# Kernel optimization log

Hardware: AMD Instinct MI355X
Metric: run time of the kernel (lower is better)

The kernel has to match this reference:

```python
import jax, jax.numpy as jnp
import numpy as np


def setup_inputs() -> dict:
    key = jax.random.key(0)
    k1, k2 = jax.random.split(key)
    B, N, d = 8, 4096, 256
    S_pred = jax.random.normal(k1, (B, N, d), dtype=jnp.float32)
    # binary adjacency in {0,1}; nonzero entries define neighbors
    adjacency = jax.random.randint(k2, (N, N), 0, 2, dtype=jnp.int32)
    return {"S_pred": S_pred, "adjacency": adjacency}


def reference(S_pred, adjacency):
    # S_pred: (B, N, d), adjacency: (N, N)
    B, N, d = S_pred.shape
    A = (adjacency != 0).astype(S_pred.dtype)          # (N, N) binary
    deg = A.sum(axis=1)                                 # (N,) neighbor counts
    # neighbor mean: (A @ S) / deg  -> per node i, mean over j in N(i) of S_j
    neigh_sum = jnp.einsum('ij,bjd->bid', A, S_pred)   # (B, N, d)
    neigh_mean = neigh_sum / jnp.maximum(deg, 1.0)[None, :, None]
    # div_i = mean_j (S_j - S_i) = neigh_mean_i - S_i; zero for isolated nodes
    div = neigh_mean - S_pred                           # (B, N, d)
    mask = (deg > 0).astype(S_pred.dtype)[None, :, None]
    divergence = jnp.sum((div * mask) ** 2) / (B * N * d)
    return divergence
```

## Files before the change

kernel.cpp:

```cpp
#include <hip/hip_runtime.h>
#include <stdint.h>

#define N_NODES 4096
#define DMODEL  256
#define BATCH   8
#define NCOL    (BATCH * DMODEL)
#define KDIM    N_NODES
#define INV_BND (1.0f / 8388608.0f)

typedef __attribute__((ext_vector_type(8))) int   int32x8;
typedef __attribute__((ext_vector_type(4))) float f32x4;

__device__ __forceinline__ void async_load16(const void* g, void* l) {
  __builtin_amdgcn_global_load_lds(
      (const __attribute__((address_space(1))) void*)g,
      (__attribute__((address_space(3))) void*)l, 16, 0, 0);
}

__device__ __forceinline__ f32x4 mfma_mx(int32x8 a, int32x8 b, f32x4 c) {
  return __builtin_amdgcn_mfma_scale_f32_16x16x128_f8f6f4(
      a, b, c, 0, 0, 0, 0x7F7F7F7Fu, 0, 0x7F7F7F7Fu);
}

__global__ __launch_bounds__(256) void fat_prep(const int* __restrict__ adj,
                                                const float* __restrict__ S,
                                                unsigned char* __restrict__ A8,
                                                unsigned char* __restrict__ B8,
                                                float* __restrict__ w,
                                                float* __restrict__ out) {
  __shared__ float tile[64][36];
  __shared__ int wred[4];
  const int bx = blockIdx.x;
  const int t  = threadIdx.x;

  if (bx < N_NODES) {
    if (bx == 0 && t == 0) *out = 0.0f;
    const int4* arow = (const int4*)(adj + (size_t)bx * N_NODES);
    int cnt = 0;
    unsigned int b[4];
#pragma unroll
    for (int q = 0; q < 4; ++q) {
      int4 a = arow[t * 4 + q];
      unsigned int p = 0;
      p |= a.x ? 0x38u       : 0u; cnt += (a.x != 0);
      p |= a.y ? 0x3800u     : 0u; cnt += (a.y != 0);
      p |= a.z ? 0x380000u   : 0u; cnt += (a.z != 0);
      p |= a.w ? 0x38000000u : 0u; cnt += (a.w != 0);
      b[q] = p;
    }
    uint4 o; o.x = b[0]; o.y = b[1]; o.z = b[2]; o.w = b[3];
    ((uint4*)(A8 + (size_t)bx * N_NODES))[t] = o;
#pragma unroll
    for (int off = 32; off > 0; off >>= 1) cnt += __shfl_down(cnt, off);
    if ((t & 63) == 0) wred[t >> 6] = cnt;
    __syncthreads();
    if (t == 0) {
      int total = wred[0] + wred[1] + wred[2] + wred[3];
      w[bx] = (total > 0) ? (1.0f / (float)total) : 0.0f;
    }
  } else {
    const int bt = bx - N_NODES;
    const int j0 = (bt & 63) * 64;
    const int d0 = ((bt >> 6) & 7) * 32;
    const int bb = bt >> 9;
    const float* Sb = S + (size_t)bb * (N_NODES * DMODEL);

    const int c  = t & 7;
    const int jr = t >> 3;
#pragma unroll
    for (int p = 0; p < 2; ++p) {
      const int j = jr + p * 32;
      float4 v = *(const float4*)&Sb[(size_t)(j0 + j) * DMODEL + d0 + c * 4];
      *(float4*)&tile[j][c * 4] = v;
    }
    __syncthreads();

    const int dr = t >> 3;
    const int jt = (t & 7) * 8;
    int lo = __builtin_amdgcn_cvt_pk_fp8_f32(tile[jt + 0][dr], tile[jt + 1][dr], 0, false);
    lo     = __builtin_amdgcn_cvt_pk_fp8_f32(tile[jt + 2][dr], tile[jt + 3][dr], lo, true);
    int hi = __builtin_amdgcn_cvt_pk_fp8_f32(tile[jt + 4][dr], tile[jt + 5][dr], 0, false);
    hi     = __builtin_amdgcn_cvt_pk_fp8_f32(tile[jt + 6][dr], tile[jt + 7][dr], hi, true);
    uint2 o; o.x = (unsigned int)lo; o.y = (unsigned int)hi;
    *(uint2*)&B8[(size_t)(bb * DMODEL + d0 + dr) * KDIM + j0 + jt] = o;
  }
}

__global__ __launch_bounds__(512, 4) void gemm_div(const unsigned char* __restrict__ A8,
                                                   const unsigned char* __restrict__ B8,
                                                   const float* __restrict__ w,
                                                   const float* __restrict__ S,
                                                   float* __restrict__ out) {
  __shared__ unsigned char lds[65536];
  __shared__ float wsum[4];

  const int tid  = threadIdx.x;
  const int lane = tid & 63;
  const int wave = tid >> 6;
  const int grp  = wave >> 2;
  const int w4   = wave & 3;
  const int wm   = w4 >> 1;
  const int wn   = w4 & 1;
  const int l16  = lane & 15;
  const int quad = lane >> 4;

  unsigned char* As = lds + grp * 16384;
  unsigned char* Bs = lds + 32768 + grp * 16384;

  const int rowBase = blockIdx.x * 128;
  const int colBase = blockIdx.y * 128;

  const int srow = lane >> 3;
  const int kc   = ((lane & 7) ^ srow) * 16;

  f32x4 acc[4][4];
  const f32x4 zero = {0.f, 0.f, 0.f, 0.f};
#pragma unroll
  for (int i = 0; i < 4; ++i)
#pragma unroll
    for (int j = 0; j < 4; ++j) acc[i][j] = zero;

  const unsigned char* Ag = A8 + (size_t)rowBase * KDIM;
  const unsigned char* Bg = B8 + (size_t)colBase * KDIM;

  for (int k0 = grp * 128; k0 < KDIM; k0 += 256) {
#pragma unroll
    for (int c = 0; c < 4; ++c) {
      const int r = (w4 * 4 + c) * 8 + srow;
      async_load16(Ag + (size_t)r * KDIM + k0 + kc, As + (w4 * 4 + c) * 1024);
      async_load16(Bg + (size_t)r * KDIM + k0 + kc, Bs + (w4 * 4 + c) * 1024);
    }
    __syncthreads();

    int32x8 bfrag[4];
#pragma unroll
    for (int nt = 0; nt < 4; ++nt) {
      const int r = wn * 64 + nt * 16 + l16;
      const unsigned char* rp = Bs + r * 128;
      const int x = r & 7;
      int4 lo = *(const int4*)(rp + (((2 * quad)    ) ^ x) * 16);
      int4 hi = *(const int4*)(rp + (((2 * quad) | 1) ^ x) * 16);
      bfrag[nt][0] = lo.x; bfrag[nt][1] = lo.y; bfrag[nt][2] = lo.z; bfrag[nt][3] = lo.w;
      bfrag[nt][4] = hi.x; bfrag[nt][5] = hi.y; bfrag[nt][6] = hi.z; bfrag[nt][7] = hi.w;
    }
#pragma unroll
    for (int mt = 0; mt < 4; ++mt) {
      const int r = wm * 64 + mt * 16 + l16;
      const unsigned char* rp = As + r * 128;
      const int x = r & 7;
      int4 lo = *(const int4*)(rp + (((2 * quad)    ) ^ x) * 16);
      int4 hi = *(const int4*)(rp + (((2 * quad) | 1) ^ x) * 16);
      int32x8 a;
      a[0] = lo.x; a[1] = lo.y; a[2] = lo.z; a[3] = lo.w;
      a[4] = hi.x; a[5] = hi.y; a[6] = hi.z; a[7] = hi.w;
#pragma unroll
      for (int nt = 0; nt < 4; ++nt)
        acc[mt][nt] = mfma_mx(a, bfrag[nt], acc[mt][nt]);
    }
    __syncthreads();
  }

  float* stash = (float*)lds;
  if (grp == 1) {
#pragma unroll
    for (int mt = 0; mt < 4; ++mt)
#pragma unroll
      for (int nt = 0; nt < 4; ++nt)
#pragma unroll
        for (int r = 0; r < 4; ++r)
          stash[w4 * 4096 + (mt * 4 + nt) * 256 + (quad * 4 + r) * 16 + l16] =
              acc[mt][nt][r];
  }
  __syncthreads();

  float local = 0.0f;
  if (grp == 0) {
#pragma unroll
    for (int mt = 0; mt < 4; ++mt) {
      const int i0 = rowBase + wm * 64 + mt * 16 + quad * 4;
      float wr[4];
#pragma unroll
      for (int r = 0; r < 4; ++r) wr[r] = w[i0 + r];
#pragma unroll
      for (int nt = 0; nt < 4; ++nt) {
        const int col = colBase + wn * 64 + nt * 16 + l16;
        const int bb = col >> 8;
        const int dd = col & 255;
        const float* Sp = S + (size_t)bb * (N_NODES * DMODEL) + (size_t)i0 * DMODEL + dd;
#pragma unroll
        for (int r = 0; r < 4; ++r) {
          float cs = acc[mt][nt][r] +
                     stash[w4 * 4096 + (mt * 4 + nt) * 256 + (quad * 4 + r) * 16 + l16];
          float v = cs * wr[r] - Sp[(size_t)r * DMODEL];
          v = (wr[r] > 0.0f) ? v : 0.0f;
          local += v * v;
        }
      }
    }
#pragma unroll
    for (int off = 32; off > 0; off >>= 1) local += __shfl_down(local, off);
    if (lane == 0) wsum[w4] = local;
  }
  __syncthreads();
  if (tid == 0)
    atomicAdd(out, (wsum[0] + wsum[1] + wsum[2] + wsum[3]) * INV_BND);
}

extern "C" void kernel_launch(void* const* d_in, const int* in_sizes, int n_in,
                              void* d_out, int out_size, void* d_ws, size_t ws_size,
                              hipStream_t stream) {
  const float* S  = (const float*)d_in[0];
  const int* adj  = (const int*)d_in[1];
  float* out = (float*)d_out;

  unsigned char* A8 = (unsigned char*)d_ws;
  unsigned char* B8 = (unsigned char*)d_ws + (size_t)N_NODES * N_NODES;
  float* w = (float*)((char*)d_ws + (size_t)N_NODES * N_NODES + (size_t)NCOL * KDIM);

  fat_prep<<<N_NODES + N_NODES / 64 * (DMODEL / 32) * BATCH, 256, 0, stream>>>(
      adj, S, A8, B8, w, out);

  gemm_div<<<dim3(N_NODES / 128, NCOL / 128, 1), 512, 0, stream>>>(A8, B8, w, S, out);
}
```

Measured before the change: 165.3 us.

## Remove intra-block split-K in FP8 GEMM and widen prep transpose tiles

The GEMM kernel drops its two-group split-K, where 8 waves each handled half of K and the halves were reduced through LDS. It now runs 4 waves over the full K with a 32KB LDS footprint, which removes the stash write, an extra barrier and LDS usage. The prep transpose now handles 128 rows per block and writes 16-byte FP8 stores instead of 8-byte ones. In exchange, each GEMM block runs twice as many serial K iterations with fewer resident waves per CU, which can reduce latency hiding on a 512-block grid.

```diff
diff --git a/kernel.cpp b/kernel.cpp
--- a/kernel.cpp
+++ b/kernel.cpp
@@ -28,7 +28,7 @@
                                                 unsigned char* __restrict__ B8,
                                                 float* __restrict__ w,
                                                 float* __restrict__ out) {
-  __shared__ float tile[64][36];
+  __shared__ float tile[128][36];
   __shared__ int wred[4];
   const int bx = blockIdx.x;
   const int t  = threadIdx.x;
@@ -60,53 +60,57 @@
     }
   } else {
     const int bt = bx - N_NODES;
-    const int j0 = (bt & 63) * 64;
-    const int d0 = ((bt >> 6) & 7) * 32;
-    const int bb = bt >> 9;
+    const int j0 = (bt & 31) * 128;
+    const int d0 = ((bt >> 5) & 7) * 32;
+    const int bb = bt >> 8;
     const float* Sb = S + (size_t)bb * (N_NODES * DMODEL);
 
-    const int c  = t & 7;
-    const int jr = t >> 3;
-#pragma unroll
-    for (int p = 0; p < 2; ++p) {
-      const int j = jr + p * 32;
+#pragma unroll
+    for (int p = 0; p < 4; ++p) {
+      const int idx = p * 256 + t;
+      const int j = idx >> 3;
+      const int c = idx & 7;
       float4 v = *(const float4*)&Sb[(size_t)(j0 + j) * DMODEL + d0 + c * 4];
       *(float4*)&tile[j][c * 4] = v;
     }
     __syncthreads();
 
     const int dr = t >> 3;
-    const int jt = (t & 7) * 8;
-    int lo = __builtin_amdgcn_cvt_pk_fp8_f32(tile[jt + 0][dr], tile[jt + 1][dr], 0, false);
-    lo     = __builtin_amdgcn_cvt_pk_fp8_f32(tile[jt + 2][dr], tile[jt + 3][dr], lo, true);
-    int hi = __builtin_amdgcn_cvt_pk_fp8_f32(tile[jt + 4][dr], tile[jt + 5][dr], 0, false);
-    hi     = __builtin_amdgcn_cvt_pk_fp8_f32(tile[jt + 6][dr], tile[jt + 7][dr], hi, true);
-    uint2 o; o.x = (unsigned int)lo; o.y = (unsigned int)hi;
-    *(uint2*)&B8[(size_t)(bb * DMODEL + d0 + dr) * KDIM + j0 + jt] = o;
+    const int jt = (t & 7) * 16;
+    uint4 o;
+    {
+      int v0 = __builtin_amdgcn_cvt_pk_fp8_f32(tile[jt + 0][dr], tile[jt + 1][dr], 0, false);
+      v0     = __builtin_amdgcn_cvt_pk_fp8_f32(tile[jt + 2][dr], tile[jt + 3][dr], v0, true);
+      int v1 = __builtin_amdgcn_cvt_pk_fp8_f32(tile[jt + 4][dr], tile[jt + 5][dr], 0, false);
+      v1     = __builtin_amdgcn_cvt_pk_fp8_f32(tile[jt + 6][dr], tile[jt + 7][dr], v1, true);
+      int v2 = __builtin_amdgcn_cvt_pk_fp8_f32(tile[jt + 8][dr], tile[jt + 9][dr], 0, false);
+      v2     = __builtin_amdgcn_cvt_pk_fp8_f32(tile[jt +10][dr], tile[jt +11][dr], v2, true);
+      int v3 = __builtin_amdgcn_cvt_pk_fp8_f32(tile[jt +12][dr], tile[jt +13][dr], 0, false);
+      v3     = __builtin_amdgcn_cvt_pk_fp8_f32(tile[jt +14][dr], tile[jt +15][dr], v3, true);
+      o.x = (unsigned int)v0; o.y = (unsigned int)v1;
+      o.z = (unsigned int)v2; o.w = (unsigned int)v3;
+    }
+    *(uint4*)&B8[(size_t)(bb * DMODEL + d0 + dr) * KDIM + j0 + jt] = o;
   }
 }
 
-__global__ __launch_bounds__(512, 4) void gemm_div(const unsigned char* __restrict__ A8,
+__global__ __launch_bounds__(256, 4) void gemm_div(const unsigned char* __restrict__ A8,
                                                    const unsigned char* __restrict__ B8,
                                                    const float* __restrict__ w,
                                                    const float* __restrict__ S,
                                                    float* __restrict__ out) {
-  __shared__ unsigned char lds[65536];
+  __shared__ unsigned char As[16384];
+  __shared__ unsigned char Bs[16384];
   __shared__ float wsum[4];
 
   const int tid  = threadIdx.x;
   const int lane = tid & 63;
   const int wave = tid >> 6;
-  const int grp  = wave >> 2;
-  const int w4   = wave & 3;
-  const int wm   = w4 >> 1;
-  const int wn   = w4 & 1;
+  const int wm   = wave >> 1;
+  const int wn   = wave & 1;
   const int l16  = lane & 15;
   const int quad = lane >> 4;
 
-  unsigned char* As = lds + grp * 16384;
-  unsigned char* Bs = lds + 32768 + grp * 16384;
-
   const int rowBase = blockIdx.x * 128;
   const int colBase = blockIdx.y * 128;
 
@@ -123,12 +127,13 @@
   const unsigned char* Ag = A8 + (size_t)rowBase * KDIM;
   const unsigned char* Bg = B8 + (size_t)colBase * KDIM;
 
-  for (int k0 = grp * 128; k0 < KDIM; k0 += 256) {
+  for (int k0 = 0; k0 < KDIM; k0 += 128) {
 #pragma unroll
     for (int c = 0; c < 4; ++c) {
-      const int r = (w4 * 4 + c) * 8 + srow;
-      async_load16(Ag + (size_t)r * KDIM + k0 + kc, As + (w4 * 4 + c) * 1024);
-      async_load16(Bg + (size_t)r * KDIM + k0 + kc, Bs + (w4 * 4 + c) * 1024);
+      const int ch = wave * 4 + c;
+      const int r  = ch * 8 + srow;
+      async_load16(Ag + (size_t)r * KDIM + k0 + kc, As + ch * 1024);
+      async_load16(Bg + (size_t)r * KDIM + k0 + kc, Bs + ch * 1024);
     }
     __syncthreads();
 
@@ -160,47 +165,31 @@
     __syncthreads();
   }
 
-  float* stash = (float*)lds;
-  if (grp == 1) {
-#pragma unroll
-    for (int mt = 0; mt < 4; ++mt)
-#pragma unroll
-      for (int nt = 0; nt < 4; ++nt)
-#pragma unroll
-        for (int r = 0; r < 4; ++r)
-          stash[w4 * 4096 + (mt * 4 + nt) * 256 + (quad * 4 + r) * 16 + l16] =
-              acc[mt][nt][r];
+  float local = 0.0f;
+#pragma unroll
+  for (int mt = 0; mt < 4; ++mt) {
+    const int i0 = rowBase + wm * 64 + mt * 16 + quad * 4;
+    float wr[4];
+#pragma unroll
+    for (int r = 0; r < 4; ++r) wr[r] = w[i0 + r];
+#pragma unroll
+    for (int nt = 0; nt < 4; ++nt) {
+      const int col = colBase + wn * 64 + nt * 16 + l16;
+      const int bb = col >> 8;
+      const int dd = col & 255;
+      const float* Sp = S + (size_t)bb * (N_NODES * DMODEL) + (size_t)i0 * DMODEL + dd;
+#pragma unroll
+      for (int r = 0; r < 4; ++r) {
+        float v = acc[mt][nt][r] * wr[r] - Sp[(size_t)r * DMODEL];
+        v = (wr[r] > 0.0f) ? v : 0.0f;
+        local += v * v;
+      }
+    }
   }
-  __syncthreads();
-
-  float local = 0.0f;
-  if (grp == 0) {
-#pragma unroll
-    for (int mt = 0; mt < 4; ++mt) {
-      const int i0 = rowBase + wm * 64 + mt * 16 + quad * 4;
-      float wr[4];
-#pragma unroll
-      for (int r = 0; r < 4; ++r) wr[r] = w[i0 + r];
-#pragma unroll
-      for (int nt = 0; nt < 4; ++nt) {
-        const int col = colBase + wn * 64 + nt * 16 + l16;
-        const int bb = col >> 8;
-        const int dd = col & 255;
-        const float* Sp = S + (size_t)bb * (N_NODES * DMODEL) + (size_t)i0 * DMODEL + dd;
-#pragma unroll
-        for (int r = 0; r < 4; ++r) {
-          float cs = acc[mt][nt][r] +
-                     stash[w4 * 4096 + (mt * 4 + nt) * 256 + (quad * 4 + r) * 16 + l16];
-          float v = cs * wr[r] - Sp[(size_t)r * DMODEL];
-          v = (wr[r] > 0.0f) ? v : 0.0f;
-          local += v * v;
-        }
-      }
-    }
-#pragma unroll
-    for (int off = 32; off > 0; off >>= 1) local += __shfl_down(local, off);
-    if (lane == 0) wsum[w4] = local;
-  }
+
+#pragma unroll
+  for (int off = 32; off > 0; off >>= 1) local += __shfl_down(local, off);
+  if (lane == 0) wsum[wave] = local;
   __syncthreads();
   if (tid == 0)
     atomicAdd(out, (wsum[0] + wsum[1] + wsum[2] + wsum[3]) * INV_BND);
@@ -217,8 +206,8 @@
   unsigned char* B8 = (unsigned char*)d_ws + (size_t)N_NODES * N_NODES;
   float* w = (float*)((char*)d_ws + (size_t)N_NODES * N_NODES + (size_t)NCOL * KDIM);
 
-  fat_prep<<<N_NODES + N_NODES / 64 * (DMODEL / 32) * BATCH, 256, 0, stream>>>(
+  fat_prep<<<N_NODES + (N_NODES / 128) * (DMODEL / 32) * BATCH, 256, 0, stream>>>(
       adj, S, A8, B8, w, out);
 
-  gemm_div<<<dim3(N_NODES / 128, NCOL / 128, 1), 512, 0, stream>>>(A8, B8, w, S, out);
-}
+  gemm_div<<<dim3(N_NODES / 128, NCOL / 128, 1), 256, 0, stream>>>(A8, B8, w, S, out);
+}
```

Measured after the change: 163.3 us. No clear change (-1.2%).
